# Kernel optimization log

Hardware: AMD Instinct MI355X
Metric: run time of the kernel (lower is better)

## Reference

```python
import jax, jax.numpy as jnp
import numpy as np
import math
from functools import lru_cache

DIM = 64   # num_inputs
HID = 32   # hidden_dim
B = 1024
LOG2 = math.log(2.0)
LOG_2PI = math.log(2.0 * math.pi)


@lru_cache(maxsize=None)
def _masks(out_f, in_f, dim):
    ob, ib = out_f // dim, in_f // dim
    md = np.zeros((out_f, in_f), np.float32)
    mo = np.ones((out_f, in_f), np.float32)
    for i in range(dim):
        md[i * ob:(i + 1) * ob, i * ib:(i + 1) * ib] = 1.0
        mo[i * ob:(i + 1) * ob, i * ib:] = 0.0
    return jnp.asarray(md), jnp.asarray(mo)


def masked_weight(x, grad, W, dw, b, dim):
    # W: (out_f, in_f), dw: (out_f, 1), b: (out_f,)
    out_f, in_f = W.shape
    ob, ib = out_f // dim, in_f // dim
    md, mo = _masks(out_f, in_f, dim)
    w = jnp.exp(W) * md + W * mo                      # positive diag blocks, masked lower blocks
    wsn = jnp.sum(w * w, axis=-1, keepdims=True)      # (out_f, 1) weight-norm denom^2
    wn = jnp.exp(dw) * w / jnp.sqrt(wsn)              # weight-normalized matrix
    wpl = dw + W - 0.5 * jnp.log(wsn)                 # log of diag-block entries, (out_f, in_f)
    # extract diagonal blocks: (dim, ob, dim, ib) -> diag over block index -> (ob, ib, dim)
    blocks = jnp.diagonal(wpl.reshape(dim, ob, dim, ib), axis1=0, axis2=2)
    g = jnp.transpose(blocks, (2, 0, 1))              # (dim, ob, ib) == torch g per-sample
    out = x @ wn.T + b
    if grad is None:
        return out, jnp.broadcast_to(g[None], (x.shape[0],) + g.shape)
    # grad: (Bt, dim, a, c); log-domain block 'matmul' via logsumexp over shared axis a(=ib)
    comb = g[None, :, :, None, :] + jnp.swapaxes(grad, -1, -2)[:, :, None, :, :]  # (Bt,dim,ob,c,ib)
    return out, jax.nn.logsumexp(comb, axis=-1)       # (Bt, dim, ob, c)


def tanh_layer(x, grad):
    g = -2.0 * (x - LOG2 + jax.nn.softplus(-2.0 * x))
    return jnp.tanh(x), g.reshape(grad.shape) + grad


def bnaf_flow(x, p0, p1, p2, gate, dim):
    out, grad = masked_weight(x, None, *p0, dim)
    out, grad = tanh_layer(out, grad)
    out, grad = masked_weight(out, grad, *p1, dim)
    out, grad = tanh_layer(out, grad)
    out, grad = masked_weight(out, grad, *p2, dim)
    g = grad.reshape(grad.shape[0], dim)              # squeeze (B, dim, 1, 1) -> (B, dim)
    if gate is None:
        return out, jnp.sum(g, -1)
    s = jax.nn.sigmoid(gate)
    out = s * out + (1.0 - s) * x
    ldj = jnp.sum(jax.nn.softplus(g + gate) - jax.nn.softplus(gate), -1)
    return out, ldj


def _forward(x, params, gates):
    ldj = 0.0
    for f in range(3):
        gate = gates[f] if f < 2 else None
        x, l = bnaf_flow(x, params[f][0], params[f][1], params[f][2], gate, DIM)
        ldj = ldj + l
        if f < 2:
            x = x[:, ::-1]                            # Permutation('flip'), log-det 0
    log_p_y = jnp.sum(-0.5 * x * x - 0.5 * LOG_2PI, -1)
    return log_p_y + ldj                              # (B,)


def setup_inputs() -> dict:
    key = jax.random.key(0)
    ks = iter(jax.random.split(key, 64))
    d, dh = DIM, DIM * HID
    shapes = [(dh, d), (dh, dh), (d, dh)]
    inp = {"x": jax.random.normal(next(ks), (B, d), jnp.float32)}
    for f in range(3):
        for l, (o, i) in enumerate(shapes):
            inp[f"W{f}_{l}"] = 0.1 * jax.random.normal(next(ks), (o, i), jnp.float32)
            inp[f"dw{f}_{l}"] = jnp.log(jax.random.uniform(next(ks), (o, 1), jnp.float32, 0.1, 1.0))
            inp[f"b{f}_{l}"] = 0.01 * jax.random.normal(next(ks), (o,), jnp.float32)
    inp["gate0"] = jax.random.normal(next(ks), (1,), jnp.float32)
    inp["gate1"] = jax.random.normal(next(ks), (1,), jnp.float32)
    return inp


def reference(x, W0_0, dw0_0, b0_0, W0_1, dw0_1, b0_1, W0_2, dw0_2, b0_2,
              W1_0, dw1_0, b1_0, W1_1, dw1_1, b1_1, W1_2, dw1_2, b1_2,
              W2_0, dw2_0, b2_0, W2_1, dw2_1, b2_1, W2_2, dw2_2, b2_2,
              gate0, gate1):
    params = [
        [(W0_0, dw0_0, b0_0), (W0_1, dw0_1, b0_1), (W0_2, dw0_2, b0_2)],
        [(W1_0, dw1_0, b1_0), (W1_1, dw1_1, b1_1), (W1_2, dw1_2, b1_2)],
        [(W2_0, dw2_0, b2_0), (W2_1, dw2_1, b2_1), (W2_2, dw2_2, b2_2)],
    ]
    return _forward(x, params, (gate0, gate1))
```

## Files before the change

kernel.cpp:

```cpp
#include <hip/hip_runtime.h>
#include <hip/hip_bf16.h>
#include <math.h>


#define DIMN 64
#define BATCH 1024
#define HIDF 2048
#define SPLITK 2
#define NT2 32

typedef __attribute__((ext_vector_type(8))) short short8;
typedef __attribute__((ext_vector_type(4))) float floatx4;

__device__ __forceinline__ float softplusf_(float t) {
    return fmaxf(t, 0.f) + log1pf(__expf(-fabsf(t)));
}

__device__ __forceinline__ void gl_lds16(const void* g, void* l) {
    __builtin_amdgcn_global_load_lds(
        (const __attribute__((address_space(1))) unsigned int*)g,
        (__attribute__((address_space(3))) unsigned int*)l, 16, 0, 0);
}

__device__ __forceinline__ void tanh_sech2_(float p, float& th, float& s2) {
    float t = __expf(-2.f * fabsf(p));
    float opt = 1.f + t;
    float inv = 1.f / opt;
    th = copysignf((1.f - t) * inv, p);
    s2 = 4.f * t * inv * inv;
}

template<int INF>
__device__ __forceinline__ void prep_row(
    const float* __restrict__ W, const float* __restrict__ dw,
    void* __restrict__ wn_out, float* __restrict__ eg,
    int r, int lane, int out_f, int ob, int ib, int transpose, int bf16out)
{
    constexpr int NI = INF / 64;
    int d = r / ob;
    int c0 = d * ib;
    int c1 = c0 + ib;
    const float* Wr = W + (size_t)r * INF;

    float vv[NI];
    float ss = 0.f;
#pragma unroll
    for (int i = 0; i < NI; ++i) {
        int c = lane + i * 64;
        float wraw = Wr[c];
        float wv = (c < c0) ? wraw : ((c < c1) ? __expf(wraw) : 0.f);
        vv[i] = wv;
        ss += wv * wv;
    }
    for (int off = 32; off > 0; off >>= 1) ss += __shfl_xor(ss, off, 64);

    float dwr = dw[r];
    float scale = __expf(dwr) / sqrtf(ss);
    float logt = dwr - 0.5f * __logf(ss);

#pragma unroll
    for (int i = 0; i < NI; ++i) {
        int c = lane + i * 64;
        float val = scale * vv[i];
        if (bf16out) {
            ((__hip_bfloat16*)wn_out)[(size_t)r * INF + c] = __float2bfloat16(val);
        } else if (transpose) {
            ((float*)wn_out)[(size_t)c * out_f + r] = val;
        } else {
            ((float*)wn_out)[(size_t)r * INF + c] = val;
        }
    }
    if (lane < ib) eg[(size_t)r * ib + lane] = __expf(logt + Wr[c0 + lane]);
}

struct PrepIn { const float *W0, *dw0, *W1, *dw1, *W2, *dw2; };

__global__ __launch_bounds__(64) void prep_mega(
    PrepIn p0, PrepIn p1, PrepIn p2,
    float* __restrict__ wn0T_all, float* __restrict__ eg0_all,
    __hip_bfloat16* __restrict__ wn1_all, float* __restrict__ e1_all,
    __hip_bfloat16* __restrict__ wn2b_all, float* __restrict__ e2_all)
{
    int blk = blockIdx.x;
    int lane = threadIdx.x;
    int f = blk / 4160;
    int rem = blk - f * 4160;
    PrepIn P = (f == 0) ? p0 : ((f == 1) ? p1 : p2);

    float* wn0T = wn0T_all + (size_t)f * DIMN * HIDF;
    float* eg0  = eg0_all  + (size_t)f * HIDF;
    __hip_bfloat16* wn1 = wn1_all + (size_t)f * HIDF * HIDF;
    float* e1   = e1_all   + (size_t)f * HIDF * 32;
    __hip_bfloat16* wn2b = wn2b_all + (size_t)f * DIMN * HIDF;
    float* e2   = e2_all   + (size_t)f * DIMN * 32;

    if (rem < HIDF) {
        prep_row<DIMN>(P.W0, P.dw0, wn0T, eg0, rem, lane, HIDF, 32, 1, 1, 0);
    } else if (rem < 2 * HIDF) {
        prep_row<HIDF>(P.W1, P.dw1, wn1, e1, rem - HIDF, lane, HIDF, 32, 32, 0, 1);
    } else {
        prep_row<HIDF>(P.W2, P.dw2, wn2b, e2, rem - 2 * HIDF, lane, DIMN, 1, 32, 0, 1);
    }
}

__global__ __launch_bounds__(256) void gemm0_act(
    const float* __restrict__ xin, const float* __restrict__ wn0T,
    const float* __restrict__ bias, const float* __restrict__ eg0,
    __hip_bfloat16* __restrict__ h0, float* __restrict__ g0e)
{
    __shared__ float xs[16][DIMN];
    int b0 = blockIdx.y * 16;
    {
        const float4* src = (const float4*)(xin + (size_t)b0 * DIMN);
        ((float4*)xs)[threadIdx.x] = src[threadIdx.x];
    }
    __syncthreads();
    int n = blockIdx.x * 256 + threadIdx.x;

    float acc[16];
#pragma unroll
    for (int j = 0; j < 16; ++j) acc[j] = 0.f;

#pragma unroll 4
    for (int c4 = 0; c4 < 16; ++c4) {
        int c = c4 * 4;
        float w0 = wn0T[(size_t)(c + 0) * HIDF + n];
        float w1 = wn0T[(size_t)(c + 1) * HIDF + n];
        float w2 = wn0T[(size_t)(c + 2) * HIDF + n];
        float w3 = wn0T[(size_t)(c + 3) * HIDF + n];
#pragma unroll
        for (int j = 0; j < 16; ++j) {
            float4 x4 = *(const float4*)&xs[j][c];
            acc[j] = fmaf(x4.x, w0, acc[j]);
            acc[j] = fmaf(x4.y, w1, acc[j]);
            acc[j] = fmaf(x4.z, w2, acc[j]);
            acc[j] = fmaf(x4.w, w3, acc[j]);
        }
    }
    float bv = bias[n], egv = eg0[n];
#pragma unroll
    for (int j = 0; j < 16; ++j) {
        float p = acc[j] + bv;
        float th, s2;
        tanh_sech2_(p, th, s2);
        size_t idx = (size_t)(b0 + j) * HIDF + n;
        h0[idx] = __float2bfloat16(th);
        g0e[idx] = egv * s2;
    }
}

#define G1BK 64
__global__ __launch_bounds__(256) void gemm1_part(
    const __hip_bfloat16* __restrict__ A, const __hip_bfloat16* __restrict__ B,
    __hip_bfloat16* __restrict__ part)
{
    __shared__ short As[64 * 64];
    __shared__ short Bs[64 * 64];
    const int K = HIDF, N = HIDF;
    int tid = threadIdx.x;
    int lane = tid & 63;
    int wave = tid >> 6;
    int m0 = blockIdx.y * 64;
    int n0 = blockIdx.x * 64;
    int kbase = blockIdx.z * (K / SPLITK);
    int wr = wave & 1;
    int wc = wave >> 1;

    int rf = lane & 15;
    int q = lane >> 4;

    int r0c = tid >> 3,          k0c = (tid & 7) ^ (r0c & 7);
    int r1c = (tid + 256) >> 3,  k1c = (tid & 7) ^ (r1c & 7);
    const char* agp0 = (const char*)A + ((size_t)(m0 + r0c) * K + kbase) * 2 + k0c * 16;
    const char* agp1 = (const char*)A + ((size_t)(m0 + r1c) * K + kbase) * 2 + k1c * 16;
    const char* bgp0 = (const char*)B + ((size_t)(n0 + r0c) * K + kbase) * 2 + k0c * 16;
    const char* bgp1 = (const char*)B + ((size_t)(n0 + r1c) * K + kbase) * 2 + k1c * 16;
    char* alds0 = (char*)As + tid * 16;
    char* alds1 = (char*)As + 4096 + tid * 16;
    char* blds0 = (char*)Bs + tid * 16;
    char* blds1 = (char*)Bs + 4096 + tid * 16;

    floatx4 acc[2][2];
#pragma unroll
    for (int i = 0; i < 2; ++i)
#pragma unroll
        for (int j = 0; j < 2; ++j) acc[i][j] = (floatx4){0.f, 0.f, 0.f, 0.f};

    int rowA0 = wr * 32 + rf;
    int rowB0 = wc * 32 + rf;

    for (int k0 = 0; k0 < K / SPLITK; k0 += G1BK) {
        size_t kb = (size_t)k0 * 2;
        __syncthreads();
        gl_lds16(agp0 + kb, alds0);
        gl_lds16(agp1 + kb, alds1);
        gl_lds16(bgp0 + kb, blds0);
        gl_lds16(bgp1 + kb, blds1);
        __syncthreads();

#pragma unroll
        for (int s = 0; s < 2; ++s) {
            short8 af0, af1, bf0, bf1;
            {
                int row = rowA0;
                af0 = *(const short8*)&As[row * 64 + (((s * 4 + q) ^ (row & 7)) * 8)];
                row = rowA0 + 16;
                af1 = *(const short8*)&As[row * 64 + (((s * 4 + q) ^ (row & 7)) * 8)];
                row = rowB0;
                bf0 = *(const short8*)&Bs[row * 64 + (((s * 4 + q) ^ (row & 7)) * 8)];
                row = rowB0 + 16;
                bf1 = *(const short8*)&Bs[row * 64 + (((s * 4 + q) ^ (row & 7)) * 8)];
            }
            acc[0][0] = __builtin_amdgcn_mfma_f32_16x16x32_bf16(af0, bf0, acc[0][0], 0, 0, 0);
            acc[0][1] = __builtin_amdgcn_mfma_f32_16x16x32_bf16(af0, bf1, acc[0][1], 0, 0, 0);
            acc[1][0] = __builtin_amdgcn_mfma_f32_16x16x32_bf16(af1, bf0, acc[1][0], 0, 0, 0);
            acc[1][1] = __builtin_amdgcn_mfma_f32_16x16x32_bf16(af1, bf1, acc[1][1], 0, 0, 0);
        }
    }

    __hip_bfloat16* pk = part + (size_t)blockIdx.z * BATCH * HIDF;
    int col = lane & 15;
    int rq = (lane >> 4) * 4;
#pragma unroll
    for (int i = 0; i < 2; ++i) {
#pragma unroll
        for (int j = 0; j < 2; ++j) {
            int n = n0 + wc * 32 + j * 16 + col;
#pragma unroll
            for (int r = 0; r < 4; ++r) {
                int m = m0 + wr * 32 + i * 16 + rq + r;
                pk[(size_t)m * N + n] = __float2bfloat16(acc[i][j][r]);
            }
        }
    }
}

__global__ __launch_bounds__(256) void act_grad_gemm2(
    const __hip_bfloat16* __restrict__ part, const float* __restrict__ bias,
    const float* __restrict__ e1, const float* __restrict__ g0e,
    const __hip_bfloat16* __restrict__ wn2b,
    float* __restrict__ grad1e, float* __restrict__ out2p)
{
    __shared__ char smem[17408 + 8704 + 8192];
    float* g0s = (float*)smem;
    short* h1s = (short*)(smem + 17408);
    short* Bs2 = (short*)(smem + 17408 + 8704);

    int tid = threadIdx.x;
    int lane = tid & 63;
    int wave = tid >> 6;
    int n0 = blockIdx.x * 64;
    int b0 = blockIdx.y * 64;

    {
        int c0c = tid, c1c = tid + 256;
        int r0 = c0c >> 3, k0c = (c0c & 7) ^ (r0 & 7);
        int r1 = c1c >> 3, k1c = (c1c & 7) ^ (r1 & 7);
        gl_lds16((const char*)wn2b + ((size_t)r0 * HIDF + n0) * 2 + k0c * 16,
                 (char*)Bs2 + c0c * 16);
        gl_lds16((const char*)wn2b + ((size_t)r1 * HIDF + n0) * 2 + k1c * 16,
                 (char*)Bs2 + c1c * 16);
    }

#pragma unroll
    for (int s = tid; s < 1024; s += 256) {
        int row = s >> 4, c4 = s & 15;
        *(float4*)&g0s[row * 68 + c4 * 4] =
            *(const float4*)&g0e[(size_t)(b0 + row) * HIDF + n0 + c4 * 4];
    }

    int g = tid >> 6;
    int nl = tid & 63;
    int n = n0 + nl;

    float4 er[8];
    const float4* e1r = (const float4*)(e1 + (size_t)n * 32);
#pragma unroll
    for (int qq = 0; qq < 8; ++qq) er[qq] = e1r[qq];

    float bv = bias[n];
    int kb2 = nl & 32;
    const __hip_bfloat16* p0 = part;
    const __hip_bfloat16* p1 = part + (size_t)BATCH * HIDF;

    __syncthreads();

#pragma unroll
    for (int t = 0; t < 16; ++t) {
        int bl = g * 16 + t;
        int b = b0 + bl;
        size_t idx = (size_t)b * HIDF + n;
        float pre = __bfloat162float(p0[idx]) + __bfloat162float(p1[idx]) + bv;
        float th, s2;
        tanh_sech2_(pre, th, s2);
        const float* g0row = &g0s[bl * 68 + kb2];
        float dot = 0.f;
#pragma unroll
        for (int qq = 0; qq < 8; ++qq) {
            float4 gv = *(const float4*)&g0row[qq * 4];
            dot = fmaf(gv.x, er[qq].x, dot);
            dot = fmaf(gv.y, er[qq].y, dot);
            dot = fmaf(gv.z, er[qq].z, dot);
            dot = fmaf(gv.w, er[qq].w, dot);
        }
        __hip_bfloat16 thb = __float2bfloat16(th);
        h1s[bl * 68 + nl] = *(const short*)&thb;
        grad1e[idx] = dot * s2;
    }
    __syncthreads();

    int rf = lane & 15;
    int q = lane >> 4;
    floatx4 acc2[4];
#pragma unroll
    for (int j = 0; j < 4; ++j) acc2[j] = (floatx4){0.f, 0.f, 0.f, 0.f};

#pragma unroll
    for (int s = 0; s < 2; ++s) {
        int rowa = wave * 16 + rf;
        short8 af = *(const short8*)&h1s[rowa * 68 + s * 32 + q * 8];
#pragma unroll
        for (int j = 0; j < 4; ++j) {
            int rowb = j * 16 + rf;
            int cp = (s * 4 + q) ^ (rowb & 7);
            short8 bfv = *(const short8*)&Bs2[rowb * 64 + cp * 8];
            acc2[j] = __builtin_amdgcn_mfma_f32_16x16x32_bf16(af, bfv, acc2[j], 0, 0, 0);
        }
    }

    float* outk = out2p + (size_t)blockIdx.x * BATCH * DIMN;
    int col = lane & 15;
    int rq = (lane >> 4) * 4;
#pragma unroll
    for (int j = 0; j < 4; ++j) {
#pragma unroll
        for (int r = 0; r < 4; ++r) {
            int m = b0 + wave * 16 + rq + r;
            outk[(size_t)m * DIMN + j * 16 + col] = acc2[j][r];
        }
    }
}

__global__ __launch_bounds__(256) void tail_trans(
    const float* __restrict__ out2p, const float* __restrict__ b2,
    const float* __restrict__ e2, const float* __restrict__ grad1e,
    const float* __restrict__ x_cur, const float* __restrict__ gate,
    float* __restrict__ x_next, float* __restrict__ ldj, int accum_ldj)
{
    int tid = threadIdx.x;
    int b = blockIdx.x * 4 + (tid >> 6);
    int n = tid & 63;

    float o = b2[n];
#pragma unroll
    for (int p = 0; p < NT2; ++p)
        o += out2p[(size_t)p * BATCH * DIMN + (size_t)b * DIMN + n];

    float gt = gate[0];
    float sg = 1.f / (1.f + __expf(-gt));
    float xo = sg * o + (1.f - sg) * x_cur[(size_t)b * DIMN + n];
    x_next[(size_t)b * DIMN + (63 - n)] = xo;

    const float4* gr = (const float4*)(grad1e + (size_t)b * HIDF + n * 32);
    const float4* gc = (const float4*)(e2 + n * 32);
    float s = 0.f;
#pragma unroll
    for (int q = 0; q < 8; ++q) {
        float4 a = gr[q], c = gc[q];
        s = fmaf(a.x, c.x, s);
        s = fmaf(a.y, c.y, s);
        s = fmaf(a.z, c.z, s);
        s = fmaf(a.w, c.w, s);
    }
    float gF = __logf(fmaxf(s, 1e-45f));
    float contrib = softplusf_(gF + gt) - softplusf_(gt);
    for (int off = 32; off > 0; off >>= 1) contrib += __shfl_xor(contrib, off, 64);
    if (n == 0) ldj[b] = accum_ldj ? (ldj[b] + contrib) : contrib;
}

__global__ __launch_bounds__(256) void tail_final(
    const float* __restrict__ out2p, const float* __restrict__ b2,
    const float* __restrict__ e2, const float* __restrict__ grad1e,
    const float* __restrict__ ldj, float* __restrict__ out)
{
    int tid = threadIdx.x;
    int b = blockIdx.x * 4 + (tid >> 6);
    int n = tid & 63;

    float o = b2[n];
#pragma unroll
    for (int p = 0; p < NT2; ++p)
        o += out2p[(size_t)p * BATCH * DIMN + (size_t)b * DIMN + n];

    const float4* gr = (const float4*)(grad1e + (size_t)b * HIDF + n * 32);
    const float4* gc = (const float4*)(e2 + n * 32);
    float s = 0.f;
#pragma unroll
    for (int q = 0; q < 8; ++q) {
        float4 a = gr[q], c = gc[q];
        s = fmaf(a.x, c.x, s);
        s = fmaf(a.y, c.y, s);
        s = fmaf(a.z, c.z, s);
        s = fmaf(a.w, c.w, s);
    }
    float gF = __logf(fmaxf(s, 1e-45f));

    float contrib = gF - 0.5f * o * o - 0.91893853320467274f;
    for (int off = 32; off > 0; off >>= 1) contrib += __shfl_xor(contrib, off, 64);
    if (n == 0) out[b] = ldj[b] + contrib;
}

extern "C" void kernel_launch(void* const* d_in, const int* in_sizes, int n_in,
                              void* d_out, int out_size, void* d_ws, size_t ws_size,
                              hipStream_t stream)
{
    (void)in_sizes; (void)n_in; (void)out_size; (void)ws_size;

    const float* x = (const float*)d_in[0];
    const float* gates[2] = { (const float*)d_in[28], (const float*)d_in[29] };

    char* ws = (char*)d_ws;
    size_t ofs = 0;
    auto alloc = [&](size_t bytes) { char* p = ws + ofs; ofs += (bytes + 255) & ~(size_t)255; return p; };

    __hip_bfloat16* wn1_all  = (__hip_bfloat16*)alloc((size_t)3 * HIDF * HIDF * 2);
    __hip_bfloat16* wn2b_all = (__hip_bfloat16*)alloc((size_t)3 * DIMN * HIDF * 2);
    float* wn0T_all = (float*)alloc((size_t)3 * DIMN * HIDF * 4);
    float* eg0_all  = (float*)alloc((size_t)3 * HIDF * 4);
    float* e1_all   = (float*)alloc((size_t)3 * HIDF * 32 * 4);
    float* e2_all   = (float*)alloc((size_t)3 * DIMN * 32 * 4);
    __hip_bfloat16* h0   = (__hip_bfloat16*)alloc((size_t)BATCH * HIDF * 2);
    __hip_bfloat16* part = (__hip_bfloat16*)alloc((size_t)SPLITK * BATCH * HIDF * 2);
    float* g0e    = (float*)alloc((size_t)BATCH * HIDF * 4);
    float* grad1e = (float*)alloc((size_t)BATCH * HIDF * 4);
    float* out2p  = (float*)alloc((size_t)NT2 * BATCH * DIMN * 4);
    float* x1     = (float*)alloc((size_t)BATCH * DIMN * 4);
    float* x2     = (float*)alloc((size_t)BATCH * DIMN * 4);
    float* ldj    = (float*)alloc(BATCH * 4);
    float* outp   = (float*)d_out;

    auto W = [&](int f, int i) { return (const float*)d_in[1 + f * 9 + i]; };

    PrepIn p0 = { W(0,0), W(0,1), W(0,3), W(0,4), W(0,6), W(0,7) };
    PrepIn p1 = { W(1,0), W(1,1), W(1,3), W(1,4), W(1,6), W(1,7) };
    PrepIn p2 = { W(2,0), W(2,1), W(2,3), W(2,4), W(2,6), W(2,7) };

    prep_mega<<<dim3(3 * 4160), dim3(64), 0, stream>>>(
        p0, p1, p2, wn0T_all, eg0_all, wn1_all, e1_all, wn2b_all, e2_all);

    gemm0_act<<<dim3(8, BATCH / 16), dim3(256), 0, stream>>>(
        x, wn0T_all, W(0,2), eg0_all, h0, g0e);

    const float* xcur = x;
    float* xnexts[2] = { x1, x2 };

    for (int f = 0; f < 3; ++f) {
        size_t fo1 = (size_t)f * HIDF * HIDF;
        size_t fo2 = (size_t)f * DIMN * HIDF;

        gemm1_part<<<dim3(HIDF / 64, BATCH / 64, SPLITK), dim3(256), 0, stream>>>(
            h0, wn1_all + fo1, part);

        act_grad_gemm2<<<dim3(HIDF / 64, BATCH / 64), dim3(256), 0, stream>>>(
            part, W(f,5), e1_all + (size_t)f * HIDF * 32, g0e,
            wn2b_all + fo2, grad1e, out2p);

        if (f < 2) {
            tail_trans<<<dim3(BATCH / 4), dim3(256), 0, stream>>>(
                out2p, W(f,8), e2_all + (size_t)f * DIMN * 32, grad1e,
                xcur, gates[f], xnexts[f], ldj, f);

            gemm0_act<<<dim3(8, BATCH / 16), dim3(256), 0, stream>>>(
                xnexts[f], wn0T_all + (size_t)(f + 1) * DIMN * HIDF, W(f + 1, 2),
                eg0_all + (size_t)(f + 1) * HIDF, h0, g0e);

            xcur = xnexts[f];
        } else {
            tail_final<<<dim3(BATCH / 4), dim3(256), 0, stream>>>(
                out2p, W(2,8), e2_all + (size_t)2 * DIMN * 32, grad1e, ldj, outp);
        }
    }
}
```

Measured before the change: 297.7 us.

## Enlarge gemm1 tiles to 128x128 with split-K 4 and store intermediates as bf16

The hidden-layer GEMM now uses 128x128 output tiles, with a 4x4 grid of MFMA accumulators per wave, to raise data reuse from LDS. Split-K rises to 4 so the grid keeps enough blocks, and the consumer sums all the partial buffers. Separately, the g0e and grad1e intermediates are stored as bf16 instead of fp32, halving their memory traffic. The bf16 storage lowers the precision of the log-det gradient terms. The extra split-K partials add write and read traffic.

New measurement: 291.4 us. -2.1%, faster.

```diff
diff --git a/kernel.cpp b/kernel.cpp
--- a/kernel.cpp
+++ b/kernel.cpp
@@ -6,7 +6,7 @@
 #define DIMN 64
 #define BATCH 1024
 #define HIDF 2048
-#define SPLITK 2
+#define SPLITK 4
 #define NT2 32
 
 typedef __attribute__((ext_vector_type(8))) short short8;
@@ -14,6 +14,12 @@
 
 __device__ __forceinline__ float softplusf_(float t) {
     return fmaxf(t, 0.f) + log1pf(__expf(-fabsf(t)));
+}
+
+__device__ __forceinline__ float bf2f(short v) {
+    union { unsigned u; float f; } x;
+    x.u = ((unsigned)(unsigned short)v) << 16;
+    return x.f;
 }
 
 __device__ __forceinline__ void gl_lds16(const void* g, void* l) {
@@ -106,7 +112,7 @@
 __global__ __launch_bounds__(256) void gemm0_act(
     const float* __restrict__ xin, const float* __restrict__ wn0T,
     const float* __restrict__ bias, const float* __restrict__ eg0,
-    __hip_bfloat16* __restrict__ h0, float* __restrict__ g0e)
+    __hip_bfloat16* __restrict__ h0, __hip_bfloat16* __restrict__ g0e)
 {
     __shared__ float xs[16][DIMN];
     int b0 = blockIdx.y * 16;
@@ -145,7 +151,7 @@
         tanh_sech2_(p, th, s2);
         size_t idx = (size_t)(b0 + j) * HIDF + n;
         h0[idx] = __float2bfloat16(th);
-        g0e[idx] = egv * s2;
+        g0e[idx] = __float2bfloat16(egv * s2);
     }
 }
 
@@ -154,67 +160,73 @@
     const __hip_bfloat16* __restrict__ A, const __hip_bfloat16* __restrict__ B,
     __hip_bfloat16* __restrict__ part)
 {
-    __shared__ short As[64 * 64];
-    __shared__ short Bs[64 * 64];
+    __shared__ short As[128 * 64];
+    __shared__ short Bs[128 * 64];
     const int K = HIDF, N = HIDF;
     int tid = threadIdx.x;
     int lane = tid & 63;
     int wave = tid >> 6;
-    int m0 = blockIdx.y * 64;
-    int n0 = blockIdx.x * 64;
+    int n0 = blockIdx.x * 128;
+    int m0 = blockIdx.y * 128;
     int kbase = blockIdx.z * (K / SPLITK);
-    int wr = wave & 1;
-    int wc = wave >> 1;
+    int wr = wave >> 1;
+    int wc = wave & 1;
 
     int rf = lane & 15;
     int q = lane >> 4;
 
-    int r0c = tid >> 3,          k0c = (tid & 7) ^ (r0c & 7);
-    int r1c = (tid + 256) >> 3,  k1c = (tid & 7) ^ (r1c & 7);
-    const char* agp0 = (const char*)A + ((size_t)(m0 + r0c) * K + kbase) * 2 + k0c * 16;
-    const char* agp1 = (const char*)A + ((size_t)(m0 + r1c) * K + kbase) * 2 + k1c * 16;
-    const char* bgp0 = (const char*)B + ((size_t)(n0 + r0c) * K + kbase) * 2 + k0c * 16;
-    const char* bgp1 = (const char*)B + ((size_t)(n0 + r1c) * K + kbase) * 2 + k1c * 16;
-    char* alds0 = (char*)As + tid * 16;
-    char* alds1 = (char*)As + 4096 + tid * 16;
-    char* blds0 = (char*)Bs + tid * 16;
-    char* blds1 = (char*)Bs + 4096 + tid * 16;
-
-    floatx4 acc[2][2];
-#pragma unroll
-    for (int i = 0; i < 2; ++i)
-#pragma unroll
-        for (int j = 0; j < 2; ++j) acc[i][j] = (floatx4){0.f, 0.f, 0.f, 0.f};
-
-    int rowA0 = wr * 32 + rf;
-    int rowB0 = wc * 32 + rf;
+    const char* agp[4];
+    const char* bgp[4];
+    char* alds[4];
+    char* blds[4];
+#pragma unroll
+    for (int s = 0; s < 4; ++s) {
+        int c = tid + s * 256;
+        int row = c >> 3;
+        int kc = (c & 7) ^ (row & 7);
+        agp[s] = (const char*)A + ((size_t)(m0 + row) * K + kbase) * 2 + kc * 16;
+        bgp[s] = (const char*)B + ((size_t)(n0 + row) * K + kbase) * 2 + kc * 16;
+        alds[s] = (char*)As + c * 16;
+        blds[s] = (char*)Bs + c * 16;
+    }
+
+    floatx4 acc[4][4];
+#pragma unroll
+    for (int i = 0; i < 4; ++i)
+#pragma unroll
+        for (int j = 0; j < 4; ++j) acc[i][j] = (floatx4){0.f, 0.f, 0.f, 0.f};
+
+    int rowA0 = wr * 64 + rf;
+    int rowB0 = wc * 64 + rf;
 
     for (int k0 = 0; k0 < K / SPLITK; k0 += G1BK) {
         size_t kb = (size_t)k0 * 2;
         __syncthreads();
-        gl_lds16(agp0 + kb, alds0);
-        gl_lds16(agp1 + kb, alds1);
-        gl_lds16(bgp0 + kb, blds0);
-        gl_lds16(bgp1 + kb, blds1);
+#pragma unroll
+        for (int s = 0; s < 4; ++s) {
+            gl_lds16(agp[s] + kb, alds[s]);
+            gl_lds16(bgp[s] + kb, blds[s]);
+        }
         __syncthreads();
 
 #pragma unroll
         for (int s = 0; s < 2; ++s) {
-            short8 af0, af1, bf0, bf1;
-            {
-                int row = rowA0;
-                af0 = *(const short8*)&As[row * 64 + (((s * 4 + q) ^ (row & 7)) * 8)];
-                row = rowA0 + 16;
-                af1 = *(const short8*)&As[row * 64 + (((s * 4 + q) ^ (row & 7)) * 8)];
-                row = rowB0;
-                bf0 = *(const short8*)&Bs[row * 64 + (((s * 4 + q) ^ (row & 7)) * 8)];
-                row = rowB0 + 16;
-                bf1 = *(const short8*)&Bs[row * 64 + (((s * 4 + q) ^ (row & 7)) * 8)];
+            short8 af[4], bfv[4];
+#pragma unroll
+            for (int i = 0; i < 4; ++i) {
+                int row = rowA0 + i * 16;
+                af[i] = *(const short8*)&As[row * 64 + (((s * 4 + q) ^ (row & 7)) * 8)];
             }
-            acc[0][0] = __builtin_amdgcn_mfma_f32_16x16x32_bf16(af0, bf0, acc[0][0], 0, 0, 0);
-            acc[0][1] = __builtin_amdgcn_mfma_f32_16x16x32_bf16(af0, bf1, acc[0][1], 0, 0, 0);
-            acc[1][0] = __builtin_amdgcn_mfma_f32_16x16x32_bf16(af1, bf0, acc[1][0], 0, 0, 0);
-            acc[1][1] = __builtin_amdgcn_mfma_f32_16x16x32_bf16(af1, bf1, acc[1][1], 0, 0, 0);
+#pragma unroll
+            for (int j = 0; j < 4; ++j) {
+                int row = rowB0 + j * 16;
+                bfv[j] = *(const short8*)&Bs[row * 64 + (((s * 4 + q) ^ (row & 7)) * 8)];
+            }
+#pragma unroll
+            for (int i = 0; i < 4; ++i)
+#pragma unroll
+                for (int j = 0; j < 4; ++j)
+                    acc[i][j] = __builtin_amdgcn_mfma_f32_16x16x32_bf16(af[i], bfv[j], acc[i][j], 0, 0, 0);
         }
     }
 
@@ -222,13 +234,13 @@
     int col = lane & 15;
     int rq = (lane >> 4) * 4;
 #pragma unroll
-    for (int i = 0; i < 2; ++i) {
-#pragma unroll
-        for (int j = 0; j < 2; ++j) {
-            int n = n0 + wc * 32 + j * 16 + col;
+    for (int i = 0; i < 4; ++i) {
+#pragma unroll
+        for (int j = 0; j < 4; ++j) {
+            int n = n0 + wc * 64 + j * 16 + col;
 #pragma unroll
             for (int r = 0; r < 4; ++r) {
-                int m = m0 + wr * 32 + i * 16 + rq + r;
+                int m = m0 + wr * 64 + i * 16 + rq + r;
                 pk[(size_t)m * N + n] = __float2bfloat16(acc[i][j][r]);
             }
         }
@@ -237,9 +249,9 @@
 
 __global__ __launch_bounds__(256) void act_grad_gemm2(
     const __hip_bfloat16* __restrict__ part, const float* __restrict__ bias,
-    const float* __restrict__ e1, const float* __restrict__ g0e,
+    const float* __restrict__ e1, const __hip_bfloat16* __restrict__ g0e,
     const __hip_bfloat16* __restrict__ wn2b,
-    float* __restrict__ grad1e, float* __restrict__ out2p)
+    __hip_bfloat16* __restrict__ grad1e, float* __restrict__ out2p)
 {
     __shared__ char smem[17408 + 8704 + 8192];
     float* g0s = (float*)smem;
@@ -262,11 +274,14 @@
                  (char*)Bs2 + c1c * 16);
     }
 
-#pragma unroll
-    for (int s = tid; s < 1024; s += 256) {
-        int row = s >> 4, c4 = s & 15;
-        *(float4*)&g0s[row * 68 + c4 * 4] =
-            *(const float4*)&g0e[(size_t)(b0 + row) * HIDF + n0 + c4 * 4];
+    for (int s = tid; s < 512; s += 256) {
+        int row = s >> 3, c8 = s & 7;
+        short8 v = *(const short8*)((const short*)g0e +
+                                    (size_t)(b0 + row) * HIDF + n0 + c8 * 8);
+        float4 lo = { bf2f(v[0]), bf2f(v[1]), bf2f(v[2]), bf2f(v[3]) };
+        float4 hi = { bf2f(v[4]), bf2f(v[5]), bf2f(v[6]), bf2f(v[7]) };
+        *(float4*)&g0s[row * 68 + c8 * 8] = lo;
+        *(float4*)&g0s[row * 68 + c8 * 8 + 4] = hi;
     }
 
     int g = tid >> 6;
@@ -280,8 +295,6 @@
 
     float bv = bias[n];
     int kb2 = nl & 32;
-    const __hip_bfloat16* p0 = part;
-    const __hip_bfloat16* p1 = part + (size_t)BATCH * HIDF;
 
     __syncthreads();
 
@@ -290,7 +303,10 @@
         int bl = g * 16 + t;
         int b = b0 + bl;
         size_t idx = (size_t)b * HIDF + n;
-        float pre = __bfloat162float(p0[idx]) + __bfloat162float(p1[idx]) + bv;
+        float pre = bv;
+#pragma unroll
+        for (int p = 0; p < SPLITK; ++p)
+            pre += __bfloat162float(part[(size_t)p * BATCH * HIDF + idx]);
         float th, s2;
         tanh_sech2_(pre, th, s2);
         const float* g0row = &g0s[bl * 68 + kb2];
@@ -305,7 +321,7 @@
         }
         __hip_bfloat16 thb = __float2bfloat16(th);
         h1s[bl * 68 + nl] = *(const short*)&thb;
-        grad1e[idx] = dot * s2;
+        grad1e[idx] = __float2bfloat16(dot * s2);
     }
     __syncthreads();
 
@@ -343,7 +359,7 @@
 
 __global__ __launch_bounds__(256) void tail_trans(
     const float* __restrict__ out2p, const float* __restrict__ b2,
-    const float* __restrict__ e2, const float* __restrict__ grad1e,
+    const float* __restrict__ e2, const __hip_bfloat16* __restrict__ grad1e,
     const float* __restrict__ x_cur, const float* __restrict__ gate,
     float* __restrict__ x_next, float* __restrict__ ldj, int accum_ldj)
 {
@@ -361,16 +377,21 @@
     float xo = sg * o + (1.f - sg) * x_cur[(size_t)b * DIMN + n];
     x_next[(size_t)b * DIMN + (63 - n)] = xo;
 
-    const float4* gr = (const float4*)(grad1e + (size_t)b * HIDF + n * 32);
+    const short8* gr = (const short8*)((const short*)grad1e + (size_t)b * HIDF + n * 32);
     const float4* gc = (const float4*)(e2 + n * 32);
     float s = 0.f;
 #pragma unroll
-    for (int q = 0; q < 8; ++q) {
-        float4 a = gr[q], c = gc[q];
-        s = fmaf(a.x, c.x, s);
-        s = fmaf(a.y, c.y, s);
-        s = fmaf(a.z, c.z, s);
-        s = fmaf(a.w, c.w, s);
+    for (int q = 0; q < 4; ++q) {
+        short8 a8 = gr[q];
+        float4 c0 = gc[2 * q], c1 = gc[2 * q + 1];
+        s = fmaf(bf2f(a8[0]), c0.x, s);
+        s = fmaf(bf2f(a8[1]), c0.y, s);
+        s = fmaf(bf2f(a8[2]), c0.z, s);
+        s = fmaf(bf2f(a8[3]), c0.w, s);
+        s = fmaf(bf2f(a8[4]), c1.x, s);
+        s = fmaf(bf2f(a8[5]), c1.y, s);
+        s = fmaf(bf2f(a8[6]), c1.z, s);
+        s = fmaf(bf2f(a8[7]), c1.w, s);
     }
     float gF = __logf(fmaxf(s, 1e-45f));
     float contrib = softplusf_(gF + gt) - softplusf_(gt);
@@ -380,7 +401,7 @@
 
 __global__ __launch_bounds__(256) void tail_final(
     const float* __restrict__ out2p, const float* __restrict__ b2,
-    const float* __restrict__ e2, const float* __restrict__ grad1e,
+    const float* __restrict__ e2, const __hip_bfloat16* __restrict__ grad1e,
     const float* __restrict__ ldj, float* __restrict__ out)
 {
     int tid = threadIdx.x;
@@ -392,16 +413,21 @@
     for (int p = 0; p < NT2; ++p)
         o += out2p[(size_t)p * BATCH * DIMN + (size_t)b * DIMN + n];
 
-    const float4* gr = (const float4*)(grad1e + (size_t)b * HIDF + n * 32);
+    const short8* gr = (const short8*)((const short*)grad1e + (size_t)b * HIDF + n * 32);
     const float4* gc = (const float4*)(e2 + n * 32);
     float s = 0.f;
 #pragma unroll
-    for (int q = 0; q < 8; ++q) {
-        float4 a = gr[q], c = gc[q];
-        s = fmaf(a.x, c.x, s);
-        s = fmaf(a.y, c.y, s);
-        s = fmaf(a.z, c.z, s);
-        s = fmaf(a.w, c.w, s);
+    for (int q = 0; q < 4; ++q) {
+        short8 a8 = gr[q];
+        float4 c0 = gc[2 * q], c1 = gc[2 * q + 1];
+        s = fmaf(bf2f(a8[0]), c0.x, s);
+        s = fmaf(bf2f(a8[1]), c0.y, s);
+        s = fmaf(bf2f(a8[2]), c0.z, s);
+        s = fmaf(bf2f(a8[3]), c0.w, s);
+        s = fmaf(bf2f(a8[4]), c1.x, s);
+        s = fmaf(bf2f(a8[5]), c1.y, s);
+        s = fmaf(bf2f(a8[6]), c1.z, s);
+        s = fmaf(bf2f(a8[7]), c1.w, s);
     }
     float gF = __logf(fmaxf(s, 1e-45f));
 
@@ -431,8 +457,8 @@
     float* e2_all   = (float*)alloc((size_t)3 * DIMN * 32 * 4);
     __hip_bfloat16* h0   = (__hip_bfloat16*)alloc((size_t)BATCH * HIDF * 2);
     __hip_bfloat16* part = (__hip_bfloat16*)alloc((size_t)SPLITK * BATCH * HIDF * 2);
-    float* g0e    = (float*)alloc((size_t)BATCH * HIDF * 4);
-    float* grad1e = (float*)alloc((size_t)BATCH * HIDF * 4);
+    __hip_bfloat16* g0e    = (__hip_bfloat16*)alloc((size_t)BATCH * HIDF * 2);
+    __hip_bfloat16* grad1e = (__hip_bfloat16*)alloc((size_t)BATCH * HIDF * 2);
     float* out2p  = (float*)alloc((size_t)NT2 * BATCH * DIMN * 4);
     float* x1     = (float*)alloc((size_t)BATCH * DIMN * 4);
     float* x2     = (float*)alloc((size_t)BATCH * DIMN * 4);
@@ -458,7 +484,7 @@
         size_t fo1 = (size_t)f * HIDF * HIDF;
         size_t fo2 = (size_t)f * DIMN * HIDF;
 
-        gemm1_part<<<dim3(HIDF / 64, BATCH / 64, SPLITK), dim3(256), 0, stream>>>(
+        gemm1_part<<<dim3(HIDF / 128, BATCH / 128, SPLITK), dim3(256), 0, stream>>>(
             h0, wn1_all + fo1, part);
 
         act_grad_gemm2<<<dim3(HIDF / 64, BATCH / 64), dim3(256), 0, stream>>>(
```
